# Kernel tuning notes

Hardware: AMD Instinct MI355X
Metric: run time of the kernel (lower is better)

The kernel has to match this reference:

```python
import jax, jax.numpy as jnp
import numpy as np

B, T, D = 2, 2048, 2048
H, G = 16, 4          # query heads, kv groups (GQA)
DK = D // H           # 128
THETA = 10000.0


def _rope(x, pos):
    # x: (B, h, T, dk); half-split rotary embedding
    dk = x.shape[-1]
    inv_freq = 1.0 / (THETA ** (jnp.arange(0, dk // 2, dtype=jnp.float32) * 2.0 / dk))
    ang = pos.astype(jnp.float32)[:, None] * inv_freq[None, :]   # (T, dk/2)
    cos, sin = jnp.cos(ang), jnp.sin(ang)                        # (T, dk/2)
    x1, x2 = x[..., : dk // 2], x[..., dk // 2 :]
    return jnp.concatenate([x1 * cos - x2 * sin, x2 * cos + x1 * sin], axis=-1)


def setup_inputs() -> dict:
    key = jax.random.key(0)
    ks = jax.random.split(key, 5)
    scale = D ** -0.5
    x = jax.random.normal(ks[0], (B, T, D), jnp.float32)
    Wq = jax.random.normal(ks[1], (D, H * DK), jnp.float32) * scale
    Wk = jax.random.normal(ks[2], (D, G * DK), jnp.float32) * scale
    Wv = jax.random.normal(ks[3], (D, G * DK), jnp.float32) * scale
    Wo = jax.random.normal(ks[4], (D, D), jnp.float32) * scale
    mask = jnp.tril(jnp.ones((T, T), dtype=bool))   # causal mask, True = attend
    pos = jnp.arange(T, dtype=jnp.int32)
    return {"x": x, "Wq": Wq, "Wk": Wk, "Wv": Wv, "Wo": Wo, "mask": mask, "pos": pos}


def reference(x, Wq, Wk, Wv, Wo, mask, pos):
    b, t, d = x.shape
    # projections (bias-free linears)
    q = (x @ Wq).reshape(b, t, H, DK).transpose(0, 2, 1, 3)   # (b, h, t, dk)
    k = (x @ Wk).reshape(b, t, G, DK).transpose(0, 2, 1, 3)   # (b, g, t, dk)
    v = (x @ Wv).reshape(b, t, G, DK).transpose(0, 2, 1, 3)
    # RoPE on q and k (module applies rope_q(q,q) and rope_k(k,k))
    q = _rope(q, pos)
    k = _rope(k, pos)
    # GQA: repeat_interleave kv heads to match query heads
    rf = H // G
    k = jnp.repeat(k, rf, axis=1)   # (b, h, t, dk)
    v = jnp.repeat(v, rf, axis=1)
    # scores + causal mask + softmax
    att = jnp.einsum('bhtd,bhTd->bhtT', q, k) / np.float32(np.sqrt(DK))
    att = jnp.where(mask[None, None, :, :], att, -jnp.inf)
    att = jax.nn.softmax(att, axis=-1)
    y = jnp.einsum('bhtT,bhTd->bhtd', att, v)
    y = y.transpose(0, 2, 1, 3).reshape(b, t, d)
    return y @ Wo
```

## Files before the change

### kernel.cpp

```cpp
#include <hip/hip_runtime.h>
#include <cstdint>
#include <cmath>


#define GLOBAL_AS __attribute__((address_space(1)))
#define LDS_AS __attribute__((address_space(3)))

typedef __bf16 bf16x8 __attribute__((ext_vector_type(8)));
typedef __bf16 bf16x4 __attribute__((ext_vector_type(4)));
typedef float f32x4 __attribute__((ext_vector_type(4)));

constexpr int Tn = 2048;

__device__ __forceinline__ f32x4 mfma_bf16(bf16x8 a, bf16x8 b, f32x4 c) {
  return __builtin_amdgcn_mfma_f32_16x16x32_bf16(a, b, c, 0, 0, 0);
}

__global__ __launch_bounds__(256) void convert_f32_bf16(const float* __restrict__ src,
                                                        __bf16* __restrict__ dst,
                                                        size_t n4) {
  const size_t i = (size_t)blockIdx.x * 256 + threadIdx.x;
  if (i >= n4) return;
  const f32x4 v = ((const f32x4*)src)[i];
  bf16x4 o;
#pragma unroll
  for (int k = 0; k < 4; ++k) o[k] = (__bf16)v[k];
  ((bf16x4*)dst)[i] = o;
}

__global__ __launch_bounds__(256) void transpose_f32_bf16(const float* __restrict__ src,
                                                          __bf16* __restrict__ dst,
                                                          int K, int N) {
  __shared__ __bf16 tile[32][33];
  const int n0 = blockIdx.x * 32, k0 = blockIdx.y * 32;
  const int tx = threadIdx.x, ty = threadIdx.y;
#pragma unroll
  for (int i = 0; i < 32; i += 8)
    tile[ty + i][tx] = (__bf16)src[(size_t)(k0 + ty + i) * N + n0 + tx];
  __syncthreads();
#pragma unroll
  for (int i = 0; i < 32; i += 8)
    dst[(size_t)(n0 + ty + i) * K + k0 + tx] = tile[tx][ty + i];
}

__global__ __launch_bounds__(256) void transpose_v(const __bf16* __restrict__ qkv,
                                                   __bf16* __restrict__ vtg) {
  __shared__ __bf16 tile[32][33];
  const int bg = blockIdx.z;
  const int b = bg >> 2, g = bg & 3;
  const int key0 = blockIdx.x * 32, d0 = blockIdx.y * 32;
  const int tx = threadIdx.x, ty = threadIdx.y;
  const __bf16* src = qkv + (size_t)b * Tn * 3072 + 2560 + g * 128;
  __bf16* dst = vtg + (size_t)bg * 128 * Tn;
#pragma unroll
  for (int i = 0; i < 32; i += 8)
    tile[ty + i][tx] = src[(size_t)(key0 + ty + i) * 3072 + d0 + tx];
  __syncthreads();
#pragma unroll
  for (int i = 0; i < 32; i += 8)
    dst[(size_t)(d0 + ty + i) * Tn + key0 + tx] = tile[tx][ty + i];
}

__global__ __launch_bounds__(256) void gemm_bt(const __bf16* __restrict__ A,
                                               const __bf16* __restrict__ BT,
                                               void* __restrict__ C,
                                               int K, int ldc, int outf32) {
  __shared__ __attribute__((aligned(16))) __bf16 As[128 * 32];
  __shared__ __attribute__((aligned(16))) __bf16 Bs[128 * 32];
  const int tid = threadIdx.x;
  const int wave = tid >> 6, lane = tid & 63;
  const int lr = lane & 15, lq = lane >> 4;
  const int wm = wave >> 1, wn = wave & 1;
  const int m0 = blockIdx.y * 128, n0 = blockIdx.x * 128;

  f32x4 acc[4][4] = {};

  const int srow = tid >> 2;
  const int scol = (tid & 3) * 8;
  const __bf16* ga = A + (size_t)(m0 + srow) * K + scol;
  const __bf16* gb = BT + (size_t)(n0 + srow) * K + scol;

  for (int kt = 0; kt < K; kt += 32) {
    __syncthreads();
#pragma unroll
    for (int it = 0; it < 2; ++it) {
      __builtin_amdgcn_global_load_lds((GLOBAL_AS void*)(ga + (size_t)it * 64 * K + kt),
                                       (LDS_AS void*)(As + it * 2048 + wave * 512), 16, 0, 0);
      __builtin_amdgcn_global_load_lds((GLOBAL_AS void*)(gb + (size_t)it * 64 * K + kt),
                                       (LDS_AS void*)(Bs + it * 2048 + wave * 512), 16, 0, 0);
    }
    __syncthreads();

    bf16x8 af[4], bfv[4];
#pragma unroll
    for (int i = 0; i < 4; ++i)
      af[i] = *(const bf16x8*)(As + (wm * 64 + i * 16 + lr) * 32 + lq * 8);
#pragma unroll
    for (int j = 0; j < 4; ++j)
      bfv[j] = *(const bf16x8*)(Bs + (wn * 64 + j * 16 + lr) * 32 + lq * 8);
#pragma unroll
    for (int i = 0; i < 4; ++i)
#pragma unroll
      for (int j = 0; j < 4; ++j)
        acc[i][j] = mfma_bf16(af[i], bfv[j], acc[i][j]);
  }

#pragma unroll
  for (int i = 0; i < 4; ++i) {
    const int row = m0 + wm * 64 + i * 16 + lq * 4;
#pragma unroll
    for (int j = 0; j < 4; ++j) {
      const int col = n0 + wn * 64 + j * 16 + lr;
#pragma unroll
      for (int r = 0; r < 4; ++r) {
        if (outf32)
          ((float*)C)[(size_t)(row + r) * ldc + col] = acc[i][j][r];
        else
          ((__bf16*)C)[(size_t)(row + r) * ldc + col] = (__bf16)acc[i][j][r];
      }
    }
  }
}

__global__ __launch_bounds__(256) void rope_kernel(__bf16* __restrict__ qkv) {
  const int row = blockIdx.x;
  const int t = row & (Tn - 1);
  for (int p = threadIdx.x; p < 1280; p += 256) {
    const int d = p & 63;
    const int hh = p >> 6;
    const int col = (hh < 16) ? (hh * 128 + d) : (2048 + (hh - 16) * 128 + d);
    const float inv = exp2f((float)d * (-13.287712379549449f / 64.f));
    const float ang = (float)t * inv;
    float sn, cs;
    __sincosf(ang, &sn, &cs);
    __bf16* ptr = qkv + (size_t)row * 3072 + col;
    const float x1 = (float)ptr[0];
    const float x2 = (float)ptr[64];
    ptr[0] = (__bf16)(x1 * cs - x2 * sn);
    ptr[64] = (__bf16)(x2 * cs + x1 * sn);
  }
}

constexpr int KVB = 64;
__global__ __launch_bounds__(256, 4) void flash_attn(const __bf16* __restrict__ qkv,
                                                     const __bf16* __restrict__ vtg,
                                                     __bf16* __restrict__ y) {
  const int b = blockIdx.y >> 4, h = blockIdx.y & 15;
  const int g = h >> 2;
  const int q0 = ((int)gridDim.x - 1 - (int)blockIdx.x) * 64;
  const int tid = threadIdx.x;
  const int wave = tid >> 6, lane = tid & 63;
  const int lr = lane & 15, lq = lane >> 4;

  const __bf16* Qb = qkv + (size_t)b * Tn * 3072 + h * 128;
  const __bf16* Kb = qkv + (size_t)b * Tn * 3072 + 2048 + g * 128;
  const __bf16* Vt = vtg + (size_t)(b * 4 + g) * 128 * Tn;

  __shared__ __attribute__((aligned(16))) __bf16 Ks[8192];
  __shared__ __attribute__((aligned(16))) __bf16 Vs[8192];
  __shared__ __attribute__((aligned(16))) __bf16 Pl[4][1024];

  const __bf16* ksrc[4];
  const __bf16* vsrc[4];
#pragma unroll
  for (int i = 0; i < 4; ++i) {
    ksrc[i] = Kb + (size_t)(i * 16 + lr) * 3072 + wave * 32 + lq * 8;
    vsrc[i] = Vt + (size_t)((i * 2 + (wave >> 1)) * 16 + lr) * Tn + (wave & 1) * 32 + lq * 8;
  }

  const int qrow = q0 + wave * 16 + lr;
  bf16x8 qf[4];
#pragma unroll
  for (int f = 0; f < 4; ++f)
    qf[f] = *(const bf16x8*)(Qb + (size_t)qrow * 3072 + f * 32 + lq * 8);

  f32x4 o[8] = {};
  float m_i[4], l_i[4];
#pragma unroll
  for (int r = 0; r < 4; ++r) { m_i[r] = -1e30f; l_i[r] = 0.f; }
  const float kscale = 0.12752909695983215f;

  __bf16* Plw = &Pl[wave][0];
  const int lr7 = lr & 7, lrh = lr >> 3;
  const int pbase = lq * 32 + lr7;

  for (int kt = 0; kt < q0 + 64; kt += KVB) {
    __syncthreads();
#pragma unroll
    for (int i = 0; i < 4; ++i) {
      __builtin_amdgcn_global_load_lds((GLOBAL_AS void*)ksrc[i],
                                       (LDS_AS void*)(Ks + (i * 256 + wave * 64) * 8), 16, 0, 0);
      __builtin_amdgcn_global_load_lds((GLOBAL_AS void*)vsrc[i],
                                       (LDS_AS void*)(Vs + (i * 256 + wave * 64) * 8), 16, 0, 0);
      ksrc[i] += (size_t)KVB * 3072;
      vsrc[i] += KVB;
    }
    __syncthreads();

    f32x4 s[4] = {};
    __builtin_amdgcn_s_setprio(1);
#pragma unroll
    for (int sub = 0; sub < 4; ++sub)
#pragma unroll
      for (int f = 0; f < 4; ++f) {
        const bf16x8 kf = *(const bf16x8*)(Ks + ((sub * 4 + f) * 64 + lane) * 8);
        s[sub] = mfma_bf16(qf[f], kf, s[sub]);
      }
    __builtin_amdgcn_s_setprio(0);

    const bool full = (kt + KVB - 1) <= (q0 + wave * 16);
    float mx[4];
    bool need = false;
#pragma unroll
    for (int r = 0; r < 4; ++r) {
      if (full) {
#pragma unroll
        for (int c = 0; c < 4; ++c) s[c][r] = s[c][r] * kscale;
      } else {
        const int q = q0 + wave * 16 + lq * 4 + r;
#pragma unroll
        for (int c = 0; c < 4; ++c)
          s[c][r] = (kt + c * 16 + lr <= q) ? s[c][r] * kscale : -1e30f;
      }
      float m = fmaxf(fmaxf(s[0][r], s[1][r]), fmaxf(s[2][r], s[3][r]));
      m = fmaxf(m, __shfl_xor(m, 1));
      m = fmaxf(m, __shfl_xor(m, 2));
      m = fmaxf(m, __shfl_xor(m, 4));
      m = fmaxf(m, __shfl_xor(m, 8));
      mx[r] = m;
      need = need || (m > m_i[r] + 8.f);
    }
    if (__any(need)) {
#pragma unroll
      for (int r = 0; r < 4; ++r) {
        const float mnew = fmaxf(m_i[r], mx[r]);
        const float alpha = __builtin_amdgcn_exp2f(m_i[r] - mnew);
        m_i[r] = mnew;
        l_i[r] *= alpha;
#pragma unroll
        for (int n = 0; n < 8; ++n) o[n][r] *= alpha;
      }
    }
#pragma unroll
    for (int r = 0; r < 4; ++r) {
#pragma unroll
      for (int c = 0; c < 4; ++c) {
        const float pv = __builtin_amdgcn_exp2f(s[c][r] - m_i[r]);
        l_i[r] += pv;
        Plw[(c >> 1) * 512 + ((c & 1) * 2 + lrh) * 128 + pbase + r * 8] = (__bf16)pv;
      }
    }

    __threadfence_block();

    const bf16x8 pa0 = *(const bf16x8*)(Plw + lane * 8);
    const bf16x8 pa1 = *(const bf16x8*)(Plw + (64 + lane) * 8);
    __builtin_amdgcn_s_setprio(1);
#pragma unroll
    for (int n = 0; n < 8; ++n) {
      const bf16x8 v0 = *(const bf16x8*)(Vs + ((n * 2 + 0) * 64 + lane) * 8);
      const bf16x8 v1 = *(const bf16x8*)(Vs + ((n * 2 + 1) * 64 + lane) * 8);
      o[n] = mfma_bf16(pa0, v0, o[n]);
      o[n] = mfma_bf16(pa1, v1, o[n]);
    }
    __builtin_amdgcn_s_setprio(0);
  }

#pragma unroll
  for (int r = 0; r < 4; ++r) {
    float l = l_i[r];
    l += __shfl_xor(l, 1);
    l += __shfl_xor(l, 2);
    l += __shfl_xor(l, 4);
    l += __shfl_xor(l, 8);
    const float inv = 1.0f / l;
    const int q = q0 + wave * 16 + lq * 4 + r;
#pragma unroll
    for (int n = 0; n < 8; ++n)
      y[(size_t)(b * Tn + q) * 2048 + h * 128 + n * 16 + lr] = (__bf16)(o[n][r] * inv);
  }
}

extern "C" void kernel_launch(void* const* d_in, const int* in_sizes, int n_in,
                              void* d_out, int out_size, void* d_ws, size_t ws_size,
                              hipStream_t stream) {
  (void)in_sizes; (void)n_in; (void)out_size; (void)ws_size;
  const float* x  = (const float*)d_in[0];
  const float* Wq = (const float*)d_in[1];
  const float* Wk = (const float*)d_in[2];
  const float* Wv = (const float*)d_in[3];
  const float* Wo = (const float*)d_in[4];
  float* out = (float*)d_out;

  __bf16* xb  = (__bf16*)d_ws;
  __bf16* y   = xb;
  __bf16* WT  = xb + (size_t)4096 * 2048;
  __bf16* WoT = WT;
  __bf16* VtG = WT + (size_t)2048 * 2048;
  __bf16* qkv = WT + (size_t)3072 * 2048;

  convert_f32_bf16<<<(4096 * 2048 / 4 + 255) / 256, 256, 0, stream>>>(x, xb, 4096 * 2048 / 4);
  dim3 tb(32, 8);
  transpose_f32_bf16<<<dim3(64, 64), tb, 0, stream>>>(Wq, WT, 2048, 2048);
  transpose_f32_bf16<<<dim3(16, 64), tb, 0, stream>>>(Wk, WT + (size_t)2048 * 2048, 2048, 512);
  transpose_f32_bf16<<<dim3(16, 64), tb, 0, stream>>>(Wv, WT + (size_t)2560 * 2048, 2048, 512);

  gemm_bt<<<dim3(3072 / 128, 4096 / 128), 256, 0, stream>>>(xb, WT, qkv, 2048, 3072, 0);
  rope_kernel<<<4096, 256, 0, stream>>>(qkv);

  transpose_v<<<dim3(Tn / 32, 4, 8), tb, 0, stream>>>(qkv, VtG);
  transpose_f32_bf16<<<dim3(64, 64), tb, 0, stream>>>(Wo, WoT, 2048, 2048);

  flash_attn<<<dim3(Tn / 64, 2 * 16), 256, 0, stream>>>(qkv, VtG, y);
  gemm_bt<<<dim3(2048 / 128, 4096 / 128), 256, 0, stream>>>(y, WoT, out, 2048, 2048, 1);
}
```

Baseline: 402.2 us.

## Double-buffer K/V tiles and widen flash attention blocks to 128 query rows

The flash attention kernel now uses 8 waves per block covering 128 query rows, so each K/V tile loaded into LDS is shared by twice as many queries. K and V tiles are double-buffered: the next tile is prefetched asynchronously into the alternate LDS buffer while the current one is computed, leaving one barrier per iteration instead of two. Waves whose query rows lie entirely before the current key tile skip its compute. In exchange LDS use roughly doubles, occupancy may fall, and the grid has half as many blocks, with causal imbalance inside a block.

```diff
diff --git a/kernel.cpp b/kernel.cpp
--- a/kernel.cpp
+++ b/kernel.cpp
@@ -142,12 +142,12 @@
 }
 
 constexpr int KVB = 64;
-__global__ __launch_bounds__(256, 4) void flash_attn(const __bf16* __restrict__ qkv,
+__global__ __launch_bounds__(512, 4) void flash_attn(const __bf16* __restrict__ qkv,
                                                      const __bf16* __restrict__ vtg,
                                                      __bf16* __restrict__ y) {
   const int b = blockIdx.y >> 4, h = blockIdx.y & 15;
   const int g = h >> 2;
-  const int q0 = ((int)gridDim.x - 1 - (int)blockIdx.x) * 64;
+  const int q0 = ((int)gridDim.x - 1 - (int)blockIdx.x) * 128;
   const int tid = threadIdx.x;
   const int wave = tid >> 6, lane = tid & 63;
   const int lr = lane & 15, lq = lane >> 4;
@@ -156,16 +156,16 @@
   const __bf16* Kb = qkv + (size_t)b * Tn * 3072 + 2048 + g * 128;
   const __bf16* Vt = vtg + (size_t)(b * 4 + g) * 128 * Tn;
 
-  __shared__ __attribute__((aligned(16))) __bf16 Ks[8192];
-  __shared__ __attribute__((aligned(16))) __bf16 Vs[8192];
-  __shared__ __attribute__((aligned(16))) __bf16 Pl[4][1024];
-
-  const __bf16* ksrc[4];
-  const __bf16* vsrc[4];
-#pragma unroll
-  for (int i = 0; i < 4; ++i) {
-    ksrc[i] = Kb + (size_t)(i * 16 + lr) * 3072 + wave * 32 + lq * 8;
-    vsrc[i] = Vt + (size_t)((i * 2 + (wave >> 1)) * 16 + lr) * Tn + (wave & 1) * 32 + lq * 8;
+  __shared__ __attribute__((aligned(16))) __bf16 Ks[2][8192];
+  __shared__ __attribute__((aligned(16))) __bf16 Vs[2][8192];
+  __shared__ __attribute__((aligned(16))) __bf16 Pl[8][1024];
+
+  const __bf16* ksrc[2];
+  const __bf16* vsrc[2];
+#pragma unroll
+  for (int i = 0; i < 2; ++i) {
+    ksrc[i] = Kb + (size_t)((i * 2 + (wave >> 2)) * 16 + lr) * 3072 + (wave & 3) * 32 + lq * 8;
+    vsrc[i] = Vt + (size_t)((i * 4 + (wave >> 1)) * 16 + lr) * Tn + (wave & 1) * 32 + lq * 8;
   }
 
   const int qrow = q0 + wave * 16 + lr;
@@ -184,86 +184,107 @@
   const int lr7 = lr & 7, lrh = lr >> 3;
   const int pbase = lq * 32 + lr7;
 
-  for (int kt = 0; kt < q0 + 64; kt += KVB) {
+#pragma unroll
+  for (int i = 0; i < 2; ++i) {
+    __builtin_amdgcn_global_load_lds((GLOBAL_AS void*)ksrc[i],
+                                     (LDS_AS void*)(&Ks[0][(i * 512 + wave * 64) * 8]), 16, 0, 0);
+    __builtin_amdgcn_global_load_lds((GLOBAL_AS void*)vsrc[i],
+                                     (LDS_AS void*)(&Vs[0][(i * 512 + wave * 64) * 8]), 16, 0, 0);
+    ksrc[i] += (size_t)KVB * 3072;
+    vsrc[i] += KVB;
+  }
+  __syncthreads();
+
+  const int ktend = q0 + 128;
+  int cur = 0;
+  for (int kt = 0; kt < ktend; kt += KVB) {
+    if (kt + KVB < ktend) {
+#pragma unroll
+      for (int i = 0; i < 2; ++i) {
+        __builtin_amdgcn_global_load_lds(
+            (GLOBAL_AS void*)ksrc[i],
+            (LDS_AS void*)(&Ks[cur ^ 1][(i * 512 + wave * 64) * 8]), 16, 0, 0);
+        __builtin_amdgcn_global_load_lds(
+            (GLOBAL_AS void*)vsrc[i],
+            (LDS_AS void*)(&Vs[cur ^ 1][(i * 512 + wave * 64) * 8]), 16, 0, 0);
+        ksrc[i] += (size_t)KVB * 3072;
+        vsrc[i] += KVB;
+      }
+    }
+
+    const bool active = kt <= q0 + wave * 16 + 15;
+    if (active) {
+      f32x4 s[4] = {};
+      __builtin_amdgcn_s_setprio(1);
+#pragma unroll
+      for (int sub = 0; sub < 4; ++sub)
+#pragma unroll
+        for (int f = 0; f < 4; ++f) {
+          const bf16x8 kf = *(const bf16x8*)(&Ks[cur][((sub * 4 + f) * 64 + lane) * 8]);
+          s[sub] = mfma_bf16(qf[f], kf, s[sub]);
+        }
+      __builtin_amdgcn_s_setprio(0);
+
+      const bool full = (kt + KVB - 1) <= (q0 + wave * 16);
+      float mx[4];
+      bool need = false;
+#pragma unroll
+      for (int r = 0; r < 4; ++r) {
+        if (full) {
+#pragma unroll
+          for (int c = 0; c < 4; ++c) s[c][r] = s[c][r] * kscale;
+        } else {
+          const int q = q0 + wave * 16 + lq * 4 + r;
+#pragma unroll
+          for (int c = 0; c < 4; ++c)
+            s[c][r] = (kt + c * 16 + lr <= q) ? s[c][r] * kscale : -1e30f;
+        }
+        float m = fmaxf(fmaxf(s[0][r], s[1][r]), fmaxf(s[2][r], s[3][r]));
+        m = fmaxf(m, __shfl_xor(m, 1));
+        m = fmaxf(m, __shfl_xor(m, 2));
+        m = fmaxf(m, __shfl_xor(m, 4));
+        m = fmaxf(m, __shfl_xor(m, 8));
+        mx[r] = m;
+        need = need || (m > m_i[r] + 8.f);
+      }
+      if (__any(need)) {
+#pragma unroll
+        for (int r = 0; r < 4; ++r) {
+          const float mnew = fmaxf(m_i[r], mx[r]);
+          const float alpha = __builtin_amdgcn_exp2f(m_i[r] - mnew);
+          m_i[r] = mnew;
+          l_i[r] *= alpha;
+#pragma unroll
+          for (int n = 0; n < 8; ++n) o[n][r] *= alpha;
+        }
+      }
+#pragma unroll
+      for (int r = 0; r < 4; ++r) {
+#pragma unroll
+        for (int c = 0; c < 4; ++c) {
+          const float pv = __builtin_amdgcn_exp2f(s[c][r] - m_i[r]);
+          l_i[r] += pv;
+          Plw[(c >> 1) * 512 + ((c & 1) * 2 + lrh) * 128 + pbase + r * 8] = (__bf16)pv;
+        }
+      }
+
+      __threadfence_block();
+
+      const bf16x8 pa0 = *(const bf16x8*)(Plw + lane * 8);
+      const bf16x8 pa1 = *(const bf16x8*)(Plw + (64 + lane) * 8);
+      __builtin_amdgcn_s_setprio(1);
+#pragma unroll
+      for (int n = 0; n < 8; ++n) {
+        const bf16x8 v0 = *(const bf16x8*)(&Vs[cur][((n * 2 + 0) * 64 + lane) * 8]);
+        const bf16x8 v1 = *(const bf16x8*)(&Vs[cur][((n * 2 + 1) * 64 + lane) * 8]);
+        o[n] = mfma_bf16(pa0, v0, o[n]);
+        o[n] = mfma_bf16(pa1, v1, o[n]);
+      }
+      __builtin_amdgcn_s_setprio(0);
+    }
+
     __syncthreads();
-#pragma unroll
-    for (int i = 0; i < 4; ++i) {
-      __builtin_amdgcn_global_load_lds((GLOBAL_AS void*)ksrc[i],
-                                       (LDS_AS void*)(Ks + (i * 256 + wave * 64) * 8), 16, 0, 0);
-      __builtin_amdgcn_global_load_lds((GLOBAL_AS void*)vsrc[i],
-                                       (LDS_AS void*)(Vs + (i * 256 + wave * 64) * 8), 16, 0, 0);
-      ksrc[i] += (size_t)KVB * 3072;
-      vsrc[i] += KVB;
-    }
-    __syncthreads();
-
-    f32x4 s[4] = {};
-    __builtin_amdgcn_s_setprio(1);
-#pragma unroll
-    for (int sub = 0; sub < 4; ++sub)
-#pragma unroll
-      for (int f = 0; f < 4; ++f) {
-        const bf16x8 kf = *(const bf16x8*)(Ks + ((sub * 4 + f) * 64 + lane) * 8);
-        s[sub] = mfma_bf16(qf[f], kf, s[sub]);
-      }
-    __builtin_amdgcn_s_setprio(0);
-
-    const bool full = (kt + KVB - 1) <= (q0 + wave * 16);
-    float mx[4];
-    bool need = false;
-#pragma unroll
-    for (int r = 0; r < 4; ++r) {
-      if (full) {
-#pragma unroll
-        for (int c = 0; c < 4; ++c) s[c][r] = s[c][r] * kscale;
-      } else {
-        const int q = q0 + wave * 16 + lq * 4 + r;
-#pragma unroll
-        for (int c = 0; c < 4; ++c)
-          s[c][r] = (kt + c * 16 + lr <= q) ? s[c][r] * kscale : -1e30f;
-      }
-      float m = fmaxf(fmaxf(s[0][r], s[1][r]), fmaxf(s[2][r], s[3][r]));
-      m = fmaxf(m, __shfl_xor(m, 1));
-      m = fmaxf(m, __shfl_xor(m, 2));
-      m = fmaxf(m, __shfl_xor(m, 4));
-      m = fmaxf(m, __shfl_xor(m, 8));
-      mx[r] = m;
-      need = need || (m > m_i[r] + 8.f);
-    }
-    if (__any(need)) {
-#pragma unroll
-      for (int r = 0; r < 4; ++r) {
-        const float mnew = fmaxf(m_i[r], mx[r]);
-        const float alpha = __builtin_amdgcn_exp2f(m_i[r] - mnew);
-        m_i[r] = mnew;
-        l_i[r] *= alpha;
-#pragma unroll
-        for (int n = 0; n < 8; ++n) o[n][r] *= alpha;
-      }
-    }
-#pragma unroll
-    for (int r = 0; r < 4; ++r) {
-#pragma unroll
-      for (int c = 0; c < 4; ++c) {
-        const float pv = __builtin_amdgcn_exp2f(s[c][r] - m_i[r]);
-        l_i[r] += pv;
-        Plw[(c >> 1) * 512 + ((c & 1) * 2 + lrh) * 128 + pbase + r * 8] = (__bf16)pv;
-      }
-    }
-
-    __threadfence_block();
-
-    const bf16x8 pa0 = *(const bf16x8*)(Plw + lane * 8);
-    const bf16x8 pa1 = *(const bf16x8*)(Plw + (64 + lane) * 8);
-    __builtin_amdgcn_s_setprio(1);
-#pragma unroll
-    for (int n = 0; n < 8; ++n) {
-      const bf16x8 v0 = *(const bf16x8*)(Vs + ((n * 2 + 0) * 64 + lane) * 8);
-      const bf16x8 v1 = *(const bf16x8*)(Vs + ((n * 2 + 1) * 64 + lane) * 8);
-      o[n] = mfma_bf16(pa0, v0, o[n]);
-      o[n] = mfma_bf16(pa1, v1, o[n]);
-    }
-    __builtin_amdgcn_s_setprio(0);
+    cur ^= 1;
   }
 
 #pragma unroll
@@ -311,6 +332,6 @@
   transpose_v<<<dim3(Tn / 32, 4, 8), tb, 0, stream>>>(qkv, VtG);
   transpose_f32_bf16<<<dim3(64, 64), tb, 0, stream>>>(Wo, WoT, 2048, 2048);
 
-  flash_attn<<<dim3(Tn / 64, 2 * 16), 256, 0, stream>>>(qkv, VtG, y);
+  flash_attn<<<dim3(Tn / 128, 2 * 16), 512, 0, stream>>>(qkv, VtG, y);
   gemm_bt<<<dim3(2048 / 128, 4096 / 128), 256, 0, stream>>>(y, WoT, out, 2048, 2048, 1);
 }
```

After: 388.9 us. -3.3%, faster.
